# Kernel optimization log

Measured on AMD Instinct MI355X. Metric: run time of the kernel, lower is better.

Reference implementation:

```python
import jax, jax.numpy as jnp
import numpy as np

SEGMENT_LENGTHS = (2048, 4096, 8192)
DILATION_RATES = (1, 2, 4)


def setup_inputs() -> dict:
    key = jax.random.key(0)
    kq, kk, kv = jax.random.split(key, 3)
    b, n, h, d = 1, 8192, 12, 64
    q = jax.random.normal(kq, (b, n, h, d), dtype=jnp.float32)
    k = jax.random.normal(kk, (b, n, h, d), dtype=jnp.float32)
    v = jax.random.normal(kv, (b, n, h, d), dtype=jnp.float32)
    return {"q": q, "k": k, "v": v, "is_causal": 1}


def _dilated_attention(q, k, v, is_causal):
    # q, k, v: [b, n, h, d]
    b, n, h, d = q.shape
    num_groups = len(SEGMENT_LENGTHS)
    gh = h // num_groups  # heads per group
    scale = 1.0 / jnp.sqrt(jnp.asarray(d, dtype=q.dtype))
    qt = jnp.swapaxes(q, 1, 2)  # [b, h, n, d]
    kt = jnp.swapaxes(k, 1, 2)
    vt = jnp.swapaxes(v, 1, 2)
    group_outputs = []
    for i, (s, r) in enumerate(zip(SEGMENT_LENGTHS, DILATION_RATES)):
        hs, he = i * gh, (i + 1) * gh
        nseg = n // s
        # [b, gh, nseg, s, d]
        qs = qt[:, hs:he].reshape(b, gh, nseg, s, d)
        ks = kt[:, hs:he].reshape(b, gh, nseg, s, d)
        vs = vt[:, hs:he].reshape(b, gh, nseg, s, d)
        offset = i % r
        idx = offset + r * jnp.arange(s // r)  # dilated positions within segment
        qd = qs[:, :, :, idx]  # [b, gh, nseg, s//r, d]
        kd = ks[:, :, :, idx]
        vd = vs[:, :, :, idx]
        scores = jnp.einsum("bgnqd,bgnkd->bgnqk", qd, kd) * scale
        if is_causal:
            mask = idx[:, None] >= idx[None, :]  # same dilated indices for q/k
            scores = jnp.where(mask, scores, -jnp.inf)
        attn = jax.nn.softmax(scores, axis=-1)
        od = jnp.einsum("bgnqk,bgnkd->bgnqd", attn, vd)
        # scatter back into full segment; non-dilated positions output zero
        og = jnp.zeros((b, gh, nseg, s, d), dtype=q.dtype).at[:, :, :, idx].set(od)
        group_outputs.append(og.reshape(b, gh, n, d))
    out = jnp.concatenate(group_outputs, axis=1)  # [b, h, n, d]
    return jnp.swapaxes(out, 1, 2)  # [b, n, h, d]


def reference(q, k, v, is_causal):
    return _dilated_attention(q, k, v, bool(is_causal))
```

## Files before the change

kernel.cpp:

```cpp
#include <hip/hip_runtime.h>

typedef __attribute__((ext_vector_type(8))) __bf16 bf16x8;
typedef __attribute__((ext_vector_type(4))) __bf16 bf16x4;
typedef __attribute__((ext_vector_type(2))) __bf16 bf16x2;
typedef __attribute__((ext_vector_type(4))) float f32x4;

#define LOG2E 1.44269504088896f
#define KSWZ(t) (((t) & 7) << 4)
#define VSWZ(d) ((((d) & 7) ^ (((d) >> 3) & 7)) << 4)


__device__ __forceinline__ void inst_decode(int inst, int& head, int& sstart,
                                            int& r, int& off)
{
    if (inst < 16)      { head = inst & 3;          sstart = (inst >> 2) * 2048; r = 1; off = 0; }
    else if (inst < 24) { int j = inst - 16; head = 4 + (j & 3); sstart = (j >> 2) * 4096; r = 2; off = 1; }
    else                { head = 8 + (inst - 24);   sstart = 0;                  r = 4; off = 2; }
}

__global__ __launch_bounds__(512)
void dilattn_partial(const float* __restrict__ Qg, const float* __restrict__ Kg,
                     const float* __restrict__ Vg, float* __restrict__ Og,
                     char* __restrict__ ws, const int* __restrict__ causal_p)
{
    const int bid  = blockIdx.x;
    const int unit = (bid & 7) * 140 + (bid >> 3);
    const int inst = unit / 40;
    const int u    = 39 - (unit % 40);
    int qt, c;
    if (u < 4) { qt = u; c = 0; }
    else {
        int v = u - 4;
        if (v < 8)       { qt = 4 + (v >> 1); c = v & 1; }
        else if (v < 20) { int t = v - 8; int q3 = t / 3; qt = 8 + q3; c = t - 3 * q3; }
        else             { int t = v - 20; qt = 12 + (t >> 2); c = t & 3; }
    }
    int head, sstart, r, off;
    inst_decode(inst, head, sstart, r, off);

    const int causal = *causal_p;
    int kt_begin, kt_end;
    bool direct;
    if (causal) {
        int nkt = 2 * qt + 2;
        kt_begin = c * 8;
        kt_end   = (kt_begin + 8 < nkt) ? kt_begin + 8 : nkt;
        direct   = (qt < 4);
    } else {
        if (c) return;
        kt_begin = 0; kt_end = 32; direct = true;
    }

    const int tid  = threadIdx.x;
    const int lane = tid & 63;
    const int wave = tid >> 6;
    const int l15  = lane & 15;
    const int lhi  = lane >> 4;

    __shared__ char KV[16384];
    __shared__ __bf16 P_lds[8][16 * 64];

    const int qrow_base = qt * 128 + wave * 16;
    const float qscale = 0.125f * LOG2E;
    bf16x8 qfrag[2];
    {
        int qr = qrow_base + l15;
        long qtok = sstart + off + (long)r * qr;
        const float* qp = Qg + qtok * 768 + head * 64 + lhi * 8;
#pragma unroll
        for (int dc = 0; dc < 2; dc++) {
            f32x4 a = *(const f32x4*)(qp + dc * 32);
            f32x4 b = *(const f32x4*)(qp + dc * 32 + 4);
#pragma unroll
            for (int j = 0; j < 4; j++) {
                qfrag[dc][j]     = (__bf16)(a[j] * qscale);
                qfrag[dc][4 + j] = (__bf16)(b[j] * qscale);
            }
        }
    }

    f32x4 acc[4] = {};
    float m_run = -INFINITY;
    float l_run = 0.f;

    const bool isK = (wave < 4);
    const int t2   = tid & 255;
    const int tokK = t2 >> 2, q4 = t2 & 3;
    const int tokP = t2 >> 3, d8 = (t2 & 7) * 8;

    f32x4 r0, r1, r2, r3;

#define LOAD_TILE(KT) do {                                                     \
        long tb = sstart + off + (long)r * ((KT) * 64);                        \
        if (isK) {                                                             \
            const float* p_ = Kg + (tb + (long)r * tokK) * 768 + head * 64 + q4 * 16; \
            r0 = *(const f32x4*)(p_);      r1 = *(const f32x4*)(p_ + 4);       \
            r2 = *(const f32x4*)(p_ + 8);  r3 = *(const f32x4*)(p_ + 12);      \
        } else {                                                               \
            const float* p0_ = Vg + (tb + (long)r * 2 * tokP) * 768 + head * 64 + d8; \
            const float* p1_ = p0_ + (long)r * 768;                            \
            r0 = *(const f32x4*)(p0_);     r1 = *(const f32x4*)(p0_ + 4);      \
            r2 = *(const f32x4*)(p1_);     r3 = *(const f32x4*)(p1_ + 4);      \
        }                                                                      \
    } while (0)

#define STORE_TILE() do {                                                      \
        if (isK) {                                                             \
            char* Kb_ = KV;                                                    \
            bf16x8 w0_, w1_;                                                   \
            _Pragma("unroll")                                                  \
            for (int j = 0; j < 4; j++) {                                      \
                w0_[j] = (__bf16)r0[j]; w0_[4 + j] = (__bf16)r1[j];            \
                w1_[j] = (__bf16)r2[j]; w1_[4 + j] = (__bf16)r3[j];            \
            }                                                                  \
            int kb_ = tokK * 128 + q4 * 32;                                    \
            *(bf16x8*)(Kb_ + ((kb_)      ^ KSWZ(tokK))) = w0_;                 \
            *(bf16x8*)(Kb_ + ((kb_ + 16) ^ KSWZ(tokK))) = w1_;                 \
        } else {                                                               \
            char* Vb_ = KV + 8192;                                             \
            _Pragma("unroll")                                                  \
            for (int j = 0; j < 4; j++) {                                      \
                int d_ = d8 + j;                                               \
                bf16x2 wa_; wa_[0] = (__bf16)r0[j]; wa_[1] = (__bf16)r2[j];    \
                *(bf16x2*)(Vb_ + ((d_ * 128 + tokP * 4) ^ VSWZ(d_))) = wa_;    \
                int d2_ = d8 + 4 + j;                                          \
                bf16x2 wb_; wb_[0] = (__bf16)r1[j]; wb_[1] = (__bf16)r3[j];    \
                *(bf16x2*)(Vb_ + ((d2_ * 128 + tokP * 4) ^ VSWZ(d2_))) = wb_;  \
            }                                                                  \
        }                                                                      \
    } while (0)

    LOAD_TILE(kt_begin);
    STORE_TILE();
    __syncthreads();

    for (int kt = kt_begin; kt < kt_end; kt++) {
        const bool pf = (kt + 1 < kt_end);
        if (pf) LOAD_TILE(kt + 1);

        char* Kb = KV;
        char* Vb = KV + 8192;

        f32x4 s[4];
        __builtin_amdgcn_s_setprio(1);
#pragma unroll
        for (int nt = 0; nt < 4; nt++) {
            f32x4 cc = {};
#pragma unroll
            for (int dc = 0; dc < 2; dc++) {
                int krow = nt * 16 + l15;
                const bf16x8 kf = *(const bf16x8*)(Kb +
                    ((krow * 128 + dc * 64 + lhi * 16) ^ KSWZ(krow)));
                cc = __builtin_amdgcn_mfma_f32_16x16x32_bf16(kf, qfrag[dc], cc, 0, 0, 0);
            }
            s[nt] = cc;
        }
        __builtin_amdgcn_s_setprio(0);

        if (causal && (kt >> 1) == qt) {
            const int kofs = kt * 64 - qt * 128 - wave * 16;
#pragma unroll
            for (int nt = 0; nt < 4; nt++)
#pragma unroll
                for (int reg = 0; reg < 4; reg++)
                    if (kofs + nt * 16 + lhi * 4 + reg > l15)
                        s[nt][reg] = -INFINITY;
        }

        float mt = fmaxf(fmaxf(s[0][0], s[0][1]), fmaxf(s[0][2], s[0][3]));
#pragma unroll
        for (int nt = 1; nt < 4; nt++)
            mt = fmaxf(mt, fmaxf(fmaxf(s[nt][0], s[nt][1]), fmaxf(s[nt][2], s[nt][3])));
        mt = fmaxf(mt, __shfl_xor(mt, 16));
        mt = fmaxf(mt, __shfl_xor(mt, 32));
        if (!__all(mt - m_run <= 8.0f)) {
            float mn = fmaxf(m_run, mt);
            float sc = exp2f(m_run - mn);
            l_run *= sc;
            float scr[4];
#pragma unroll
            for (int reg = 0; reg < 4; reg++) scr[reg] = __shfl(sc, lhi * 4 + reg);
#pragma unroll
            for (int dt = 0; dt < 4; dt++)
#pragma unroll
                for (int reg = 0; reg < 4; reg++) acc[dt][reg] *= scr[reg];
            m_run = mn;
        }
        float ps = 0.f;
#pragma unroll
        for (int nt = 0; nt < 4; nt++)
#pragma unroll
            for (int reg = 0; reg < 4; reg++) {
                float p = exp2f(s[nt][reg] - m_run);
                s[nt][reg] = p;
                ps += p;
            }
        ps += __shfl_xor(ps, 16);
        ps += __shfl_xor(ps, 32);
        l_run += ps;

        char* pl = (char*)P_lds[wave];
        const int rs = (l15 & 7) << 4;
#pragma unroll
        for (int nt = 0; nt < 4; nt++) {
            bf16x4 pw;
#pragma unroll
            for (int reg = 0; reg < 4; reg++) pw[reg] = (__bf16)s[nt][reg];
            *(bf16x4*)(pl + ((l15 * 128 + (nt * 16 + lhi * 4) * 2) ^ rs)) = pw;
        }

        __builtin_amdgcn_s_setprio(1);
#pragma unroll
        for (int kc = 0; kc < 2; kc++) {
            const bf16x8 pfg = *(const bf16x8*)(pl +
                ((l15 * 128 + kc * 64 + lhi * 16) ^ rs));
#pragma unroll
            for (int dt = 0; dt < 4; dt++) {
                int drow = dt * 16 + l15;
                const bf16x8 vf = *(const bf16x8*)(Vb +
                    ((drow * 128 + kc * 64 + lhi * 16) ^ VSWZ(drow)));
                acc[dt] = __builtin_amdgcn_mfma_f32_16x16x32_bf16(pfg, vf, acc[dt], 0, 0, 0);
            }
        }
        __builtin_amdgcn_s_setprio(0);

        __syncthreads();
        if (pf) {
            STORE_TILE();
            __syncthreads();
        }
    }

    if (direct) {
        float lq[4];
#pragma unroll
        for (int reg = 0; reg < 4; reg++) lq[reg] = __shfl(l_run, lhi * 4 + reg);
#pragma unroll
        for (int reg = 0; reg < 4; reg++) {
            float inv = 1.0f / lq[reg];
            int qr = qrow_base + lhi * 4 + reg;
            long tok = sstart + off + (long)r * qr;
            float* op = Og + tok * 768 + head * 64 + l15;
#pragma unroll
            for (int dt = 0; dt < 4; dt++) op[dt * 16] = acc[dt][reg] * inv;
            if (r >= 2) {
                float* z1 = op - 768;
#pragma unroll
                for (int dt = 0; dt < 4; dt++) z1[dt * 16] = 0.f;
            }
            if (r == 4) {
                float* z2 = op - 2 * 768;
                float* z3 = op + 768;
#pragma unroll
                for (int dt = 0; dt < 4; dt++) { z2[dt * 16] = 0.f; z3[dt * 16] = 0.f; }
            }
        }
    } else {
        const int b  = (qt < 8)  ? (qt - 4) * 2
                     : (qt < 12) ? 8 + (qt - 8) * 3
                     :             20 + (qt - 12) * 4;
        char* slotp = ws + (size_t)(inst * 36 + b + c) * 17408;
        __bf16* so = (__bf16*)slotp;
#pragma unroll
        for (int reg = 0; reg < 4; reg++) {
            int row = wave * 16 + lhi * 4 + reg;
#pragma unroll
            for (int dt = 0; dt < 4; dt++)
                so[row * 64 + dt * 16 + l15] = (__bf16)acc[dt][reg];
        }
        if (lhi == 0) {
            float* ml = (float*)(slotp + 16384);
            ml[wave * 16 + l15]       = m_run;
            ml[128 + wave * 16 + l15] = l_run;
        }
    }
#undef LOAD_TILE
#undef STORE_TILE
}

__global__ __launch_bounds__(256)
void dilattn_merge(const char* __restrict__ ws, float* __restrict__ Og,
                   const int* __restrict__ causal_p)
{
    if (!*causal_p) return;
    const int bid  = blockIdx.x;
    const int inst = bid / 12;
    const int qt   = 4 + bid % 12;
    int head, sstart, r, off;
    inst_decode(inst, head, sstart, r, off);

    const int nc = (2 * qt + 9) >> 3;
    const int b  = (qt < 8)  ? (qt - 4) * 2
                 : (qt < 12) ? 8 + (qt - 8) * 3
                 :             20 + (qt - 12) * 4;
    const char* base = ws + (size_t)(inst * 36 + b) * 17408;

    const int tid = threadIdx.x;
    const int row = tid >> 1;
    const int c32 = (tid & 1) * 32;

    float mv[4], lv[4];
    float m = -INFINITY;
#pragma unroll
    for (int c = 0; c < 4; c++) {
        if (c < nc) {
            const float* ml = (const float*)(base + c * 17408 + 16384);
            mv[c] = ml[row];
            lv[c] = ml[128 + row];
            m = fmaxf(m, mv[c]);
        }
    }
    float w[4];
    float L = 0.f;
#pragma unroll
    for (int c = 0; c < 4; c++) {
        if (c < nc) {
            w[c] = exp2f(mv[c] - m);
            L += w[c] * lv[c];
        }
    }
    const float invL = 1.0f / L;

    f32x4 o[8] = {};
#pragma unroll
    for (int c = 0; c < 4; c++) {
        if (c < nc) {
            const __bf16* ob = (const __bf16*)(base + c * 17408) + row * 64 + c32;
#pragma unroll
            for (int j = 0; j < 4; j++) {
                bf16x8 t = *(const bf16x8*)(ob + j * 8);
#pragma unroll
                for (int e = 0; e < 4; e++) {
                    o[j * 2][e]     += w[c] * (float)t[e];
                    o[j * 2 + 1][e] += w[c] * (float)t[4 + e];
                }
            }
        }
    }

    long tok = sstart + off + (long)r * (qt * 128 + row);
    float* og = Og + tok * 768 + head * 64 + c32;
#pragma unroll
    for (int j = 0; j < 8; j++) {
        f32x4 t;
#pragma unroll
        for (int e = 0; e < 4; e++) t[e] = o[j][e] * invL;
        *(f32x4*)(og + j * 4) = t;
    }
    const f32x4 zz = {};
    if (r >= 2) {
        float* z1 = og - 768;
#pragma unroll
        for (int j = 0; j < 8; j++) *(f32x4*)(z1 + j * 4) = zz;
    }
    if (r == 4) {
        float* z2 = og - 2 * 768;
        float* z3 = og + 768;
#pragma unroll
        for (int j = 0; j < 8; j++) { *(f32x4*)(z2 + j * 4) = zz; *(f32x4*)(z3 + j * 4) = zz; }
    }
}

extern "C" void kernel_launch(void* const* d_in, const int* in_sizes, int n_in,
                              void* d_out, int out_size, void* d_ws, size_t ws_size,
                              hipStream_t stream)
{
    const float* q = (const float*)d_in[0];
    const float* k = (const float*)d_in[1];
    const float* v = (const float*)d_in[2];
    const int* causal = (const int*)d_in[3];
    float* out = (float*)d_out;
    char* ws   = (char*)d_ws;

    dilattn_partial<<<dim3(28 * 40), dim3(512), 0, stream>>>(q, k, v, out, ws, causal);
    dilattn_merge<<<dim3(28 * 12), dim3(256), 0, stream>>>(ws, out, causal);
}
```

Before: 68.86 us.

## Process two query tiles per block and split key range into uniform chunks

Each block now handles 256 query rows (two 128-row halves) sharing each loaded K/V tile, and the causal key range is split into fixed 4-tile chunks with a triangular work enumeration, giving uniformly sized work units. The intent is to halve K/V global loads and LDS staging per query row and balance block durations. The merge kernel is reworked for up to 8 partial chunks with larger workspace slots. Register pressure doubles for accumulators and more blocks now go through the workspace merge path, which may add traffic.

```diff
diff --git a/kernel.cpp b/kernel.cpp
--- a/kernel.cpp
+++ b/kernel.cpp
@@ -24,31 +24,26 @@
                      char* __restrict__ ws, const int* __restrict__ causal_p)
 {
     const int bid  = blockIdx.x;
-    const int unit = (bid & 7) * 140 + (bid >> 3);
-    const int inst = unit / 40;
-    const int u    = 39 - (unit % 40);
-    int qt, c;
-    if (u < 4) { qt = u; c = 0; }
-    else {
-        int v = u - 4;
-        if (v < 8)       { qt = 4 + (v >> 1); c = v & 1; }
-        else if (v < 20) { int t = v - 8; int q3 = t / 3; qt = 8 + q3; c = t - 3 * q3; }
-        else             { int t = v - 20; qt = 12 + (t >> 2); c = t & 3; }
-    }
+    const int unit = (bid & 7) * 126 + (bid >> 3);
+    const int inst = unit / 36;
+    const int u    = unit % 36;
     int head, sstart, r, off;
     inst_decode(inst, head, sstart, r, off);
 
     const int causal = *causal_p;
-    int kt_begin, kt_end;
+    int qt, c, kt_begin, kt_end;
     bool direct;
     if (causal) {
-        int nkt = 2 * qt + 2;
-        kt_begin = c * 8;
-        kt_end   = (kt_begin + 8 < nkt) ? kt_begin + 8 : nkt;
-        direct   = (qt < 4);
+        int rem = u; qt = 0;
+        while (rem > qt) { rem -= qt + 1; qt++; }
+        c = rem;
+        kt_begin = c * 4; kt_end = kt_begin + 4;
+        direct = (qt == 0);
     } else {
-        if (c) return;
-        kt_begin = 0; kt_end = 32; direct = true;
+        if (u >= 32) return;
+        qt = u >> 2; c = u & 3;
+        kt_begin = c * 8; kt_end = kt_begin + 8;
+        direct = false;
     }
 
     const int tid  = threadIdx.x;
@@ -60,11 +55,12 @@
     __shared__ char KV[16384];
     __shared__ __bf16 P_lds[8][16 * 64];
 
-    const int qrow_base = qt * 128 + wave * 16;
+    const int qrb = qt * 256 + wave * 16;
     const float qscale = 0.125f * LOG2E;
-    bf16x8 qfrag[2];
-    {
-        int qr = qrow_base + l15;
+    bf16x8 qfrag[2][2];
+#pragma unroll
+    for (int h = 0; h < 2; h++) {
+        int qr = qrb + h * 128 + l15;
         long qtok = sstart + off + (long)r * qr;
         const float* qp = Qg + qtok * 768 + head * 64 + lhi * 8;
 #pragma unroll
@@ -73,15 +69,15 @@
             f32x4 b = *(const f32x4*)(qp + dc * 32 + 4);
 #pragma unroll
             for (int j = 0; j < 4; j++) {
-                qfrag[dc][j]     = (__bf16)(a[j] * qscale);
-                qfrag[dc][4 + j] = (__bf16)(b[j] * qscale);
-            }
-        }
-    }
-
-    f32x4 acc[4] = {};
-    float m_run = -INFINITY;
-    float l_run = 0.f;
+                qfrag[h][dc][j]     = (__bf16)(a[j] * qscale);
+                qfrag[h][dc][4 + j] = (__bf16)(b[j] * qscale);
+            }
+        }
+    }
+
+    f32x4 acc[2][4] = {};
+    float m_run[2] = {-INFINITY, -INFINITY};
+    float l_run[2] = {0.f, 0.f};
 
     const bool isK = (wave < 4);
     const int t2   = tid & 255;
@@ -140,89 +136,94 @@
 
         char* Kb = KV;
         char* Vb = KV + 8192;
-
-        f32x4 s[4];
-        __builtin_amdgcn_s_setprio(1);
-#pragma unroll
-        for (int nt = 0; nt < 4; nt++) {
-            f32x4 cc = {};
-#pragma unroll
-            for (int dc = 0; dc < 2; dc++) {
-                int krow = nt * 16 + l15;
-                const bf16x8 kf = *(const bf16x8*)(Kb +
-                    ((krow * 128 + dc * 64 + lhi * 16) ^ KSWZ(krow)));
-                cc = __builtin_amdgcn_mfma_f32_16x16x32_bf16(kf, qfrag[dc], cc, 0, 0, 0);
-            }
-            s[nt] = cc;
-        }
-        __builtin_amdgcn_s_setprio(0);
-
-        if (causal && (kt >> 1) == qt) {
-            const int kofs = kt * 64 - qt * 128 - wave * 16;
-#pragma unroll
-            for (int nt = 0; nt < 4; nt++)
-#pragma unroll
-                for (int reg = 0; reg < 4; reg++)
-                    if (kofs + nt * 16 + lhi * 4 + reg > l15)
-                        s[nt][reg] = -INFINITY;
-        }
-
-        float mt = fmaxf(fmaxf(s[0][0], s[0][1]), fmaxf(s[0][2], s[0][3]));
-#pragma unroll
-        for (int nt = 1; nt < 4; nt++)
-            mt = fmaxf(mt, fmaxf(fmaxf(s[nt][0], s[nt][1]), fmaxf(s[nt][2], s[nt][3])));
-        mt = fmaxf(mt, __shfl_xor(mt, 16));
-        mt = fmaxf(mt, __shfl_xor(mt, 32));
-        if (!__all(mt - m_run <= 8.0f)) {
-            float mn = fmaxf(m_run, mt);
-            float sc = exp2f(m_run - mn);
-            l_run *= sc;
-            float scr[4];
-#pragma unroll
-            for (int reg = 0; reg < 4; reg++) scr[reg] = __shfl(sc, lhi * 4 + reg);
-#pragma unroll
-            for (int dt = 0; dt < 4; dt++)
-#pragma unroll
-                for (int reg = 0; reg < 4; reg++) acc[dt][reg] *= scr[reg];
-            m_run = mn;
-        }
-        float ps = 0.f;
-#pragma unroll
-        for (int nt = 0; nt < 4; nt++)
-#pragma unroll
-            for (int reg = 0; reg < 4; reg++) {
-                float p = exp2f(s[nt][reg] - m_run);
-                s[nt][reg] = p;
-                ps += p;
-            }
-        ps += __shfl_xor(ps, 16);
-        ps += __shfl_xor(ps, 32);
-        l_run += ps;
-
         char* pl = (char*)P_lds[wave];
         const int rs = (l15 & 7) << 4;
-#pragma unroll
-        for (int nt = 0; nt < 4; nt++) {
-            bf16x4 pw;
-#pragma unroll
-            for (int reg = 0; reg < 4; reg++) pw[reg] = (__bf16)s[nt][reg];
-            *(bf16x4*)(pl + ((l15 * 128 + (nt * 16 + lhi * 4) * 2) ^ rs)) = pw;
-        }
-
-        __builtin_amdgcn_s_setprio(1);
-#pragma unroll
-        for (int kc = 0; kc < 2; kc++) {
-            const bf16x8 pfg = *(const bf16x8*)(pl +
-                ((l15 * 128 + kc * 64 + lhi * 16) ^ rs));
-#pragma unroll
-            for (int dt = 0; dt < 4; dt++) {
-                int drow = dt * 16 + l15;
-                const bf16x8 vf = *(const bf16x8*)(Vb +
-                    ((drow * 128 + kc * 64 + lhi * 16) ^ VSWZ(drow)));
-                acc[dt] = __builtin_amdgcn_mfma_f32_16x16x32_bf16(pfg, vf, acc[dt], 0, 0, 0);
-            }
-        }
-        __builtin_amdgcn_s_setprio(0);
+
+#pragma unroll
+        for (int h = 0; h < 2; h++) {
+            const int kofs = kt * 64 - (qrb + h * 128);
+            if (causal && kofs >= 16) continue;
+
+            f32x4 s[4];
+            __builtin_amdgcn_s_setprio(1);
+#pragma unroll
+            for (int nt = 0; nt < 4; nt++) {
+                f32x4 cc = {};
+#pragma unroll
+                for (int dc = 0; dc < 2; dc++) {
+                    int krow = nt * 16 + l15;
+                    const bf16x8 kf = *(const bf16x8*)(Kb +
+                        ((krow * 128 + dc * 64 + lhi * 16) ^ KSWZ(krow)));
+                    cc = __builtin_amdgcn_mfma_f32_16x16x32_bf16(kf, qfrag[h][dc], cc, 0, 0, 0);
+                }
+                s[nt] = cc;
+            }
+            __builtin_amdgcn_s_setprio(0);
+
+            if (causal && kofs > -64) {
+#pragma unroll
+                for (int nt = 0; nt < 4; nt++)
+#pragma unroll
+                    for (int reg = 0; reg < 4; reg++)
+                        if (kofs + nt * 16 + lhi * 4 + reg > l15)
+                            s[nt][reg] = -INFINITY;
+            }
+
+            float mt = fmaxf(fmaxf(s[0][0], s[0][1]), fmaxf(s[0][2], s[0][3]));
+#pragma unroll
+            for (int nt = 1; nt < 4; nt++)
+                mt = fmaxf(mt, fmaxf(fmaxf(s[nt][0], s[nt][1]), fmaxf(s[nt][2], s[nt][3])));
+            mt = fmaxf(mt, __shfl_xor(mt, 16));
+            mt = fmaxf(mt, __shfl_xor(mt, 32));
+            if (!__all(mt - m_run[h] <= 8.0f)) {
+                float mn = fmaxf(m_run[h], mt);
+                float sc = exp2f(m_run[h] - mn);
+                l_run[h] *= sc;
+                float scr[4];
+#pragma unroll
+                for (int reg = 0; reg < 4; reg++) scr[reg] = __shfl(sc, lhi * 4 + reg);
+#pragma unroll
+                for (int dt = 0; dt < 4; dt++)
+#pragma unroll
+                    for (int reg = 0; reg < 4; reg++) acc[h][dt][reg] *= scr[reg];
+                m_run[h] = mn;
+            }
+            float ps = 0.f;
+#pragma unroll
+            for (int nt = 0; nt < 4; nt++)
+#pragma unroll
+                for (int reg = 0; reg < 4; reg++) {
+                    float p = exp2f(s[nt][reg] - m_run[h]);
+                    s[nt][reg] = p;
+                    ps += p;
+                }
+            ps += __shfl_xor(ps, 16);
+            ps += __shfl_xor(ps, 32);
+            l_run[h] += ps;
+
+#pragma unroll
+            for (int nt = 0; nt < 4; nt++) {
+                bf16x4 pw;
+#pragma unroll
+                for (int reg = 0; reg < 4; reg++) pw[reg] = (__bf16)s[nt][reg];
+                *(bf16x4*)(pl + ((l15 * 128 + (nt * 16 + lhi * 4) * 2) ^ rs)) = pw;
+            }
+
+            __builtin_amdgcn_s_setprio(1);
+#pragma unroll
+            for (int kc = 0; kc < 2; kc++) {
+                const bf16x8 pfg = *(const bf16x8*)(pl +
+                    ((l15 * 128 + kc * 64 + lhi * 16) ^ rs));
+#pragma unroll
+                for (int dt = 0; dt < 4; dt++) {
+                    int drow = dt * 16 + l15;
+                    const bf16x8 vf = *(const bf16x8*)(Vb +
+                        ((drow * 128 + kc * 64 + lhi * 16) ^ VSWZ(drow)));
+                    acc[h][dt] = __builtin_amdgcn_mfma_f32_16x16x32_bf16(pfg, vf, acc[h][dt], 0, 0, 0);
+                }
+            }
+            __builtin_amdgcn_s_setprio(0);
+        }
 
         __syncthreads();
         if (pf) {
@@ -232,88 +233,92 @@
     }
 
     if (direct) {
-        float lq[4];
-#pragma unroll
-        for (int reg = 0; reg < 4; reg++) lq[reg] = __shfl(l_run, lhi * 4 + reg);
-#pragma unroll
-        for (int reg = 0; reg < 4; reg++) {
-            float inv = 1.0f / lq[reg];
-            int qr = qrow_base + lhi * 4 + reg;
-            long tok = sstart + off + (long)r * qr;
-            float* op = Og + tok * 768 + head * 64 + l15;
-#pragma unroll
-            for (int dt = 0; dt < 4; dt++) op[dt * 16] = acc[dt][reg] * inv;
-            if (r >= 2) {
-                float* z1 = op - 768;
-#pragma unroll
-                for (int dt = 0; dt < 4; dt++) z1[dt * 16] = 0.f;
-            }
-            if (r == 4) {
-                float* z2 = op - 2 * 768;
-                float* z3 = op + 768;
-#pragma unroll
-                for (int dt = 0; dt < 4; dt++) { z2[dt * 16] = 0.f; z3[dt * 16] = 0.f; }
+#pragma unroll
+        for (int h = 0; h < 2; h++) {
+            float lq[4];
+#pragma unroll
+            for (int reg = 0; reg < 4; reg++) lq[reg] = __shfl(l_run[h], lhi * 4 + reg);
+#pragma unroll
+            for (int reg = 0; reg < 4; reg++) {
+                float inv = 1.0f / lq[reg];
+                int qr = qrb + h * 128 + lhi * 4 + reg;
+                long tok = sstart + off + (long)r * qr;
+                float* op = Og + tok * 768 + head * 64 + l15;
+#pragma unroll
+                for (int dt = 0; dt < 4; dt++) op[dt * 16] = acc[h][dt][reg] * inv;
+                if (r >= 2) {
+                    float* z1 = op - 768;
+#pragma unroll
+                    for (int dt = 0; dt < 4; dt++) z1[dt * 16] = 0.f;
+                }
+                if (r == 4) {
+                    float* z2 = op - 2 * 768;
+                    float* z3 = op + 768;
+#pragma unroll
+                    for (int dt = 0; dt < 4; dt++) { z2[dt * 16] = 0.f; z3[dt * 16] = 0.f; }
+                }
             }
         }
     } else {
-        const int b  = (qt < 8)  ? (qt - 4) * 2
-                     : (qt < 12) ? 8 + (qt - 8) * 3
-                     :             20 + (qt - 12) * 4;
-        char* slotp = ws + (size_t)(inst * 36 + b + c) * 17408;
+        const int sb = causal ? (qt * (qt + 1) / 2 - 1) : qt * 4;
+        char* slotp = ws + (size_t)(inst * 35 + sb + c) * 34816;
         __bf16* so = (__bf16*)slotp;
-#pragma unroll
-        for (int reg = 0; reg < 4; reg++) {
-            int row = wave * 16 + lhi * 4 + reg;
-#pragma unroll
-            for (int dt = 0; dt < 4; dt++)
-                so[row * 64 + dt * 16 + l15] = (__bf16)acc[dt][reg];
-        }
-        if (lhi == 0) {
-            float* ml = (float*)(slotp + 16384);
-            ml[wave * 16 + l15]       = m_run;
-            ml[128 + wave * 16 + l15] = l_run;
+        float* ml = (float*)(slotp + 32768);
+#pragma unroll
+        for (int h = 0; h < 2; h++) {
+#pragma unroll
+            for (int reg = 0; reg < 4; reg++) {
+                int row = h * 128 + wave * 16 + lhi * 4 + reg;
+#pragma unroll
+                for (int dt = 0; dt < 4; dt++)
+                    so[row * 64 + dt * 16 + l15] = (__bf16)acc[h][dt][reg];
+            }
+            if (lhi == 0) {
+                int row = h * 128 + wave * 16 + l15;
+                ml[row]       = m_run[h];
+                ml[256 + row] = l_run[h];
+            }
         }
     }
 #undef LOAD_TILE
 #undef STORE_TILE
 }
 
-__global__ __launch_bounds__(256)
+__global__ __launch_bounds__(512)
 void dilattn_merge(const char* __restrict__ ws, float* __restrict__ Og,
                    const int* __restrict__ causal_p)
 {
-    if (!*causal_p) return;
+    const int causal = *causal_p;
     const int bid  = blockIdx.x;
-    const int inst = bid / 12;
-    const int qt   = 4 + bid % 12;
+    const int inst = bid >> 3;
+    const int qt   = bid & 7;
+    if (causal && qt == 0) return;
     int head, sstart, r, off;
     inst_decode(inst, head, sstart, r, off);
 
-    const int nc = (2 * qt + 9) >> 3;
-    const int b  = (qt < 8)  ? (qt - 4) * 2
-                 : (qt < 12) ? 8 + (qt - 8) * 3
-                 :             20 + (qt - 12) * 4;
-    const char* base = ws + (size_t)(inst * 36 + b) * 17408;
+    const int nc = causal ? (qt + 1) : 4;
+    const int sb = causal ? (qt * (qt + 1) / 2 - 1) : qt * 4;
+    const char* base = ws + (size_t)(inst * 35 + sb) * 34816;
 
     const int tid = threadIdx.x;
     const int row = tid >> 1;
     const int c32 = (tid & 1) * 32;
 
-    float mv[4], lv[4];
+    float mv[8], lv[8];
     float m = -INFINITY;
 #pragma unroll
-    for (int c = 0; c < 4; c++) {
+    for (int c = 0; c < 8; c++) {
         if (c < nc) {
-            const float* ml = (const float*)(base + c * 17408 + 16384);
+            const float* ml = (const float*)(base + c * 34816 + 32768);
             mv[c] = ml[row];
-            lv[c] = ml[128 + row];
+            lv[c] = ml[256 + row];
             m = fmaxf(m, mv[c]);
         }
     }
-    float w[4];
+    float w[8];
     float L = 0.f;
 #pragma unroll
-    for (int c = 0; c < 4; c++) {
+    for (int c = 0; c < 8; c++) {
         if (c < nc) {
             w[c] = exp2f(mv[c] - m);
             L += w[c] * lv[c];
@@ -323,9 +328,9 @@
 
     f32x4 o[8] = {};
 #pragma unroll
-    for (int c = 0; c < 4; c++) {
+    for (int c = 0; c < 8; c++) {
         if (c < nc) {
-            const __bf16* ob = (const __bf16*)(base + c * 17408) + row * 64 + c32;
+            const __bf16* ob = (const __bf16*)(base + c * 34816) + row * 64 + c32;
 #pragma unroll
             for (int j = 0; j < 4; j++) {
                 bf16x8 t = *(const bf16x8*)(ob + j * 8);
@@ -338,7 +343,7 @@
         }
     }
 
-    long tok = sstart + off + (long)r * (qt * 128 + row);
+    long tok = sstart + off + (long)r * (qt * 256 + row);
     float* og = Og + tok * 768 + head * 64 + c32;
 #pragma unroll
     for (int j = 0; j < 8; j++) {
@@ -372,6 +377,6 @@
     float* out = (float*)d_out;
     char* ws   = (char*)d_ws;
 
-    dilattn_partial<<<dim3(28 * 40), dim3(512), 0, stream>>>(q, k, v, out, ws, causal);
-    dilattn_merge<<<dim3(28 * 12), dim3(256), 0, stream>>>(ws, out, causal);
+    dilattn_partial<<<dim3(28 * 36), dim3(512), 0, stream>>>(q, k, v, out, ws, causal);
+    dilattn_merge<<<dim3(28 * 8), dim3(512), 0, stream>>>(ws, out, causal);
 }
```

Result: slower. 91.27 us (+32.6%).
